# Kernel optimization log

Measured on AMD Instinct MI355X. Metric: run time of the kernel, lower is better.

Reference implementation:

```python
import jax, jax.numpy as jnp
import numpy as np
import math

B, N, E, L = 64, 2048, 8192, 50
IN_DIM, HID, HEADS, R, BASES = 128, 64, 3, 5, 4
NODE_NUM = 100000


def setup_inputs() -> dict:
    key = jax.random.key(0)
    ks = jax.random.split(key, 16)
    node_ids = jax.random.randint(ks[0], (B, N), 0, NODE_NUM)
    edge_index = jax.random.randint(ks[1], (B, 2, E), 0, N)
    edge_type = jax.random.randint(ks[2], (B, E), 0, R)
    sent_ids = jax.random.randint(ks[3], (B, L), 0, N)
    # embedding table, padding_idx=0 row zeroed, init N(0, 1/input_dim)
    emb_table = jax.random.normal(ks[4], (NODE_NUM, IN_DIM), jnp.float32) / IN_DIM
    emb_table = emb_table.at[0].set(0.0)
    # RGCN basis decomposition params
    bases = jax.random.normal(ks[5], (BASES, IN_DIM, IN_DIM), jnp.float32) * (1.0 / math.sqrt(IN_DIM))
    comp = jax.random.normal(ks[6], (R, BASES), jnp.float32) * 0.5
    root_w = jax.random.normal(ks[7], (IN_DIM, IN_DIM), jnp.float32) * (1.0 / math.sqrt(IN_DIM))
    root_b = jnp.zeros((IN_DIM,), jnp.float32)
    # attention weights: 3 heads concatenated along output dim -> [IN_DIM, 3*HID]
    xav = math.sqrt(6.0 / (IN_DIM + HID))
    wq = jax.random.uniform(ks[8], (IN_DIM, HEADS * HID), jnp.float32, -xav, xav)
    wk = jax.random.uniform(ks[9], (IN_DIM, HEADS * HID), jnp.float32, -xav, xav)
    wv = jax.random.uniform(ks[10], (IN_DIM, HEADS * HID), jnp.float32, -xav, xav)
    attn_w = jax.random.normal(ks[11], (HEADS * HID, 1), jnp.float32) * 0.05
    attn_b = jnp.zeros((1,), jnp.float32)
    fc_w = jax.random.normal(ks[12], (HEADS * HID, 1), jnp.float32) * 0.05
    fc_b = jnp.zeros((1,), jnp.float32)
    return {"emb_table": emb_table, "bases": bases, "comp": comp, "root_w": root_w,
            "root_b": root_b, "wq": wq, "wk": wk, "wv": wv, "attn_w": attn_w,
            "attn_b": attn_b, "fc_w": fc_w, "fc_b": fc_b, "node_ids": node_ids,
            "edge_index": edge_index, "edge_type": edge_type, "sent_ids": sent_ids}


def _rgcn_conv(x, ei, et, W, root_w, root_b):
    # x: [N, D], ei: [2, E], et: [E], W: [R, D, D]
    src, tgt = ei[0], ei[1]
    msg = jnp.einsum('ei,eio->eo', x[src], W[et])            # [E, D]
    # per-(target, relation) mean normalization (PyG RGCNConv default)
    key = tgt * R + et
    deg = jax.ops.segment_sum(jnp.ones((et.shape[0],), x.dtype), key, num_segments=N * R)
    norm = 1.0 / jnp.maximum(deg[key], 1.0)
    agg = jax.ops.segment_sum(msg * norm[:, None], tgt, num_segments=N)  # [N, D]
    return agg + x @ root_w + root_b


def reference(emb_table, bases, comp, root_w, root_b, wq, wk, wv,
              attn_w, attn_b, fc_w, fc_b, node_ids, edge_index, edge_type, sent_ids):
    # relation weights from basis decomposition: [R, D, D]
    W = jnp.einsum('rb,bio->rio', comp, bases)
    x = emb_table[node_ids]                                   # [B, N, D]
    x_upd = jax.vmap(_rgcn_conv, in_axes=(0, 0, 0, None, None, None))(
        x, edge_index, edge_type, W, root_w, root_b)          # [B, N, D]
    X = jnp.take_along_axis(x_upd, sent_ids[:, :, None], axis=1)  # [B, L, D]
    # self-attention with head-concatenated Q/K/V (single softmax over 3*HID dims)
    Q = X @ wq                                                # [B, L, 3H]
    K = X @ wk
    V = X @ wv
    scores = jax.nn.softmax(jnp.einsum('bld,bmd->blm', Q, K) / math.sqrt(HEADS * HID), axis=-1)
    H = jnp.einsum('blm,bmd->bld', scores, V)                 # [B, L, 3H]
    attn = H @ attn_w + attn_b                                # [B, L, 1]
    pooled = jnp.sum(H * attn, axis=1)                        # [B, 3H]
    return jax.nn.sigmoid(pooled @ fc_w + fc_b)               # [B, 1]
```

## Files before the change

### kernel.cpp

```cpp
#include <hip/hip_runtime.h>
#include <math.h>

#define BDIM 64
#define NN   2048
#define EE   8192
#define LL   50
#define DD   128
#define RR   5
#define NBASES 4
#define H3   192
#define RECCAP 1024
#define KDIM 768
#define GR   8

__device__ __forceinline__ void fma4(float4& a, float s, const float4& w) {
    a.x = fmaf(s, w.x, a.x); a.y = fmaf(s, w.y, a.y);
    a.z = fmaf(s, w.z, a.z); a.w = fmaf(s, w.w, a.w);
}

__global__ __launch_bounds__(256) void precompute_all(
        const float* __restrict__ bases, const float* __restrict__ comp,
        const float* __restrict__ root_w, const float* __restrict__ wq,
        const float* __restrict__ wk, const float* __restrict__ wv,
        const float* __restrict__ attn_w, const float* __restrict__ fc_w,
        float* __restrict__ Wcat, float* __restrict__ A,
        float* __restrict__ va, float* __restrict__ vf) {
    int blk = blockIdx.x, t = threadIdx.x;
    if (blk < 384) {
        int idx = blk * 256 + t;
        int k = idx >> 7, o = idx & 127;
        if (k < DD) {
            Wcat[idx] = root_w[idx];
        } else {
            int r = (k - DD) >> 7, i = (k - DD) & 127;
            float s = 0.f;
#pragma unroll
            for (int bb = 0; bb < NBASES; ++bb)
                s += comp[r * NBASES + bb] * bases[bb * DD * DD + i * DD + o];
            Wcat[idx] = s;
        }
    } else if (blk < 512) {
        int i = blk - 384;
        __shared__ float wqs[H3];
        if (t < H3) wqs[t] = wq[i * H3 + t];
        __syncthreads();
        if (t < DD) {
            const float4* wkr = (const float4*)(wk + t * H3);
            float s = 0.f;
#pragma unroll
            for (int d4 = 0; d4 < H3 / 4; ++d4) {
                float4 v = wkr[d4];
                s += wqs[4*d4]*v.x + wqs[4*d4+1]*v.y + wqs[4*d4+2]*v.z + wqs[4*d4+3]*v.w;
            }
            A[i * DD + t] = s;
        }
    } else {
        if (t < DD) {
            const float4* wr = (const float4*)(wv + t * H3);
            float a = 0.f, f = 0.f;
#pragma unroll
            for (int d4 = 0; d4 < H3 / 4; ++d4) {
                float4 v = wr[d4];
                a += v.x*attn_w[4*d4] + v.y*attn_w[4*d4+1] + v.z*attn_w[4*d4+2] + v.w*attn_w[4*d4+3];
                f += v.x*fc_w[4*d4] + v.y*fc_w[4*d4+1] + v.z*fc_w[4*d4+2] + v.w*fc_w[4*d4+3];
            }
            va[t] = a; vf[t] = f;
        }
    }
}

__global__ __launch_bounds__(512) void matchseg(const int* __restrict__ edge_index,
                                                const int* __restrict__ edge_type,
                                                const int* __restrict__ sent_ids,
                                                int* __restrict__ rep,
                                                int* __restrict__ segoff,
                                                int* __restrict__ recbuf2) {
    int b = blockIdx.x, t = threadIdx.x;
    __shared__ int mark[NN];
    __shared__ int scnt[LL * RR];
    __shared__ int soff[LL * RR + 1];
    __shared__ int scan[256];
    __shared__ int recs[RECCAP];
    __shared__ int lcnt;

    for (int i = t; i < NN; i += 512) mark[i] = -1;
    if (t < LL * RR) scnt[t] = 0;
    if (t == 0) lcnt = 0;
    __syncthreads();
    const int* sb = sent_ids + b * LL;
    if (t < LL) mark[sb[t]] = t;
    __syncthreads();
    if (t < LL) rep[b * LL + t] = mark[sb[t]];

    const int* src_arr = edge_index + (size_t)b * 2 * EE;
    const int* tgt_arr = src_arr + EE;
    const int* et_arr  = edge_type + (size_t)b * EE;
    const int4* tgt4 = (const int4*)tgt_arr;
    for (int i4 = t; i4 < EE / 4; i4 += 512) {
        int4 v = tgt4[i4];
        int e0 = 4 * i4;
        int lv[4] = {mark[v.x], mark[v.y], mark[v.z], mark[v.w]};
#pragma unroll
        for (int k = 0; k < 4; ++k) {
            int l = lv[k];
            if (l >= 0) {
                int e = e0 + k;
                int r = et_arr[e];
                int s = src_arr[e];
                int pos = atomicAdd(&lcnt, 1);
                if (pos < RECCAP) {
                    recs[pos] = (l << 14) | (r << 11) | s;
                    atomicAdd(&scnt[l * RR + r], 1);
                }
            }
        }
    }
    __syncthreads();
    if (t < 256) scan[t] = (t < LL * RR) ? scnt[t] : 0;
    __syncthreads();
    for (int off = 1; off < 256; off <<= 1) {
        int v = 0;
        if (t < 256 && t >= off) v = scan[t - off];
        __syncthreads();
        if (t < 256) scan[t] += v;
        __syncthreads();
    }
    if (t == 0) soff[0] = 0;
    if (t < LL * RR) soff[t + 1] = scan[t];
    if (t < LL * RR) scnt[t] = 0;
    __syncthreads();
    if (t <= LL * RR) segoff[b * (LL * RR + 1) + t] = soff[t];
    int nm = (lcnt < RECCAP) ? lcnt : RECCAP;
    for (int i = t; i < nm; i += 512) {
        int rc = recs[i];
        int key = (rc >> 14) * RR + ((rc >> 11) & 7);
        int pos = soff[key] + atomicAdd(&scnt[key], 1);
        recbuf2[b * RECCAP + pos] = rc;
    }
}

__global__ __launch_bounds__(256) void gemm_fused8(const float* __restrict__ emb,
                                                   const float* __restrict__ Wcat,
                                                   const float* __restrict__ A,
                                                   const float* __restrict__ root_b,
                                                   const float* __restrict__ va,
                                                   const float* __restrict__ vf,
                                                   const int* __restrict__ node_ids,
                                                   const int* __restrict__ sent_ids,
                                                   const int* __restrict__ rep,
                                                   const int* __restrict__ segoff,
                                                   const int* __restrict__ recbuf2,
                                                   float* __restrict__ Xws,
                                                   float* __restrict__ XAws,
                                                   float* __restrict__ pv,
                                                   float* __restrict__ qv) {
    __shared__ float Us[GR][KDIM];
    __shared__ float Xs[GR][DD];
    __shared__ float vas[DD], vfs[DD];

    int t = threadIdx.x;
    int w = t >> 6, lane = t & 63;
    int row0 = blockIdx.x * GR;

#pragma unroll
    for (int rr = 0; rr < 2; ++rr) {
        int lrow = 2 * w + rr;
        int bl = row0 + lrow;
        int b  = bl / LL;
        const int* nid = node_ids + (size_t)b * NN;
        int myrep = rep[bl];
        const int* so = segoff + b * (LL * RR + 1) + myrep * RR;
        const int* rb = recbuf2 + b * RECCAP;
        int nrow = nid[sent_ids[bl]];
        Us[lrow][lane]      = emb[(size_t)nrow * DD + lane];
        Us[lrow][lane + 64] = emb[(size_t)nrow * DD + 64 + lane];
#pragma unroll
        for (int r = 0; r < RR; ++r) {
            int s0 = so[r], s1 = so[r + 1];
            float a0 = 0.f, a1 = 0.f;
            for (int j = s0; j < s1; ++j) {
                int s = rb[j] & 2047;
                int rw = nid[s];
                a0 += emb[(size_t)rw * DD + lane];
                a1 += emb[(size_t)rw * DD + 64 + lane];
            }
            float inv = (s1 > s0) ? 1.f / (float)(s1 - s0) : 0.f;
            Us[lrow][DD + r * DD + lane]      = a0 * inv;
            Us[lrow][DD + r * DD + 64 + lane] = a1 * inv;
        }
    }
    if (t < DD) { vas[t] = va[t]; vfs[t] = vf[t]; }
    __syncthreads();

    int cg = t & 31, rg = t >> 5;
    int bl_r = row0 + rg;
    float4 acc = *(const float4*)(root_b + 4 * cg);
    const float4* Wc4 = (const float4*)Wcat;
    const float4* u4p = (const float4*)Us[rg];
#pragma unroll 2
    for (int k4 = 0; k4 < KDIM / 4; ++k4) {
        float4 u = u4p[k4];
        int k = 4 * k4;
        float4 w0 = Wc4[(k + 0) * 32 + cg];
        float4 w1 = Wc4[(k + 1) * 32 + cg];
        float4 w2 = Wc4[(k + 2) * 32 + cg];
        float4 w3 = Wc4[(k + 3) * 32 + cg];
        fma4(acc, u.x, w0);
        fma4(acc, u.y, w1);
        fma4(acc, u.z, w2);
        fma4(acc, u.w, w3);
    }
    *(float4*)&Xs[rg][4 * cg] = acc;
    *(float4*)(Xws + (size_t)bl_r * DD + 4 * cg) = acc;

    float4 z = {0.f, 0.f, 0.f, 0.f};
    const float4* A4 = (const float4*)A;
    const float4* x4p = (const float4*)Xs[rg];
#pragma unroll 2
    for (int k4 = 0; k4 < DD / 4; ++k4) {
        float4 x = x4p[k4];
        int k = 4 * k4;
        float4 a0 = A4[(k + 0) * 32 + cg];
        float4 a1 = A4[(k + 1) * 32 + cg];
        float4 a2 = A4[(k + 2) * 32 + cg];
        float4 a3 = A4[(k + 3) * 32 + cg];
        fma4(z, x.x, a0);
        fma4(z, x.y, a1);
        fma4(z, x.z, a2);
        fma4(z, x.w, a3);
    }
    *(float4*)(XAws + (size_t)bl_r * DD + 4 * cg) = z;

#pragma unroll
    for (int rr = 0; rr < 2; ++rr) {
        int m = 2 * w + rr;
        float xv0 = Xs[m][lane], xv1 = Xs[m][lane + 64];
        float pp = xv0 * vas[lane] + xv1 * vas[lane + 64];
        float qq = xv0 * vfs[lane] + xv1 * vfs[lane + 64];
#pragma unroll
        for (int off = 32; off; off >>= 1) {
            pp += __shfl_xor(pp, off);
            qq += __shfl_xor(qq, off);
        }
        if (lane == 0) { pv[row0 + m] = pp; qv[row0 + m] = qq; }
    }
}

__global__ __launch_bounds__(256) void attn_batch(const float* __restrict__ Xws,
                                                  const float* __restrict__ XAws,
                                                  const float* __restrict__ pv,
                                                  const float* __restrict__ qv,
                                                  const float* __restrict__ attn_b,
                                                  const float* __restrict__ fc_b,
                                                  float* __restrict__ out) {
    __shared__ float4 XT4[32][64];
    __shared__ float4 XA4[LL][32];
    __shared__ float pvs[64], qvs[64];
    __shared__ float partial[4];

    int b = blockIdx.x, t = threadIdx.x;
    int w = t >> 6, lane = t & 63;

    const float4* Xb4  = (const float4*)(Xws  + (size_t)b * LL * DD);
    const float4* XAb4 = (const float4*)(XAws + (size_t)b * LL * DD);
    for (int idx = t; idx < LL * 32; idx += 256) {
        int m = idx >> 5, k = idx & 31;
        XT4[k][m] = Xb4[idx];
        ((float4*)XA4)[idx] = XAb4[idx];
    }
    if (t < 64) {
        pvs[t] = (t < LL) ? pv[b * LL + t] : 0.f;
        qvs[t] = (t < LL) ? qv[b * LL + t] : 0.f;
    }
    __syncthreads();

    const float scale = 0.07216878364870322f;
    float ab = attn_b[0];
    float local = 0.f;
    for (int l = w; l < LL; l += 4) {
        float s = 0.f;
#pragma unroll
        for (int kk = 0; kk < 32; ++kk) {
            float4 xa = XA4[l][kk];
            float4 xt = XT4[kk][lane];
            s = fmaf(xa.x, xt.x, s);
            s = fmaf(xa.y, xt.y, s);
            s = fmaf(xa.z, xt.z, s);
            s = fmaf(xa.w, xt.w, s);
        }
        s *= scale;
        float sval = (lane < LL) ? s : -INFINITY;
        float mx = sval;
#pragma unroll
        for (int off = 32; off; off >>= 1) mx = fmaxf(mx, __shfl_xor(mx, off));
        float e = (lane < LL) ? __expf(sval - mx) : 0.f;
        float sum = e, pa = e * pvs[lane], qa = e * qvs[lane];
#pragma unroll
        for (int off = 32; off; off >>= 1) {
            sum += __shfl_xor(sum, off);
            pa  += __shfl_xor(pa, off);
            qa  += __shfl_xor(qa, off);
        }
        float inv = 1.f / sum;
        local += (pa * inv + ab) * (qa * inv);
    }
    if (lane == 0) partial[w] = local;
    __syncthreads();
    if (t == 0) {
        float s = partial[0] + partial[1] + partial[2] + partial[3];
        out[b] = 1.f / (1.f + expf(-(s + fc_b[0])));
    }
}

extern "C" void kernel_launch(void* const* d_in, const int* in_sizes, int n_in,
                              void* d_out, int out_size, void* d_ws, size_t ws_size,
                              hipStream_t stream) {
    const float* emb     = (const float*)d_in[0];
    const float* bases   = (const float*)d_in[1];
    const float* comp    = (const float*)d_in[2];
    const float* root_w  = (const float*)d_in[3];
    const float* root_b  = (const float*)d_in[4];
    const float* wq      = (const float*)d_in[5];
    const float* wk      = (const float*)d_in[6];
    const float* wv      = (const float*)d_in[7];
    const float* attn_w  = (const float*)d_in[8];
    const float* attn_b  = (const float*)d_in[9];
    const float* fc_w    = (const float*)d_in[10];
    const float* fc_b    = (const float*)d_in[11];
    const int* node_ids  = (const int*)d_in[12];
    const int* edge_index= (const int*)d_in[13];
    const int* edge_type = (const int*)d_in[14];
    const int* sent_ids  = (const int*)d_in[15];
    float* out = (float*)d_out;

    float* ws = (float*)d_ws;
    float* Wcat = ws;
    float* A    = ws + 98304;
    float* va   = ws + 114688;
    float* vf   = ws + 114816;
    float* pv   = ws + 114944;
    float* qv   = ws + 118144;
    float* Xws  = ws + 121344;
    float* XAws = ws + 530944;
    int* rep     = (int*)(ws + 940544);
    int* segoff  = (int*)(ws + 943744);
    int* recbuf2 = (int*)(ws + 959808);

    hipLaunchKernelGGL(precompute_all, dim3(513), dim3(256), 0, stream,
                       bases, comp, root_w, wq, wk, wv, attn_w, fc_w,
                       Wcat, A, va, vf);
    hipLaunchKernelGGL(matchseg, dim3(BDIM), dim3(512), 0, stream,
                       edge_index, edge_type, sent_ids, rep, segoff, recbuf2);
    hipLaunchKernelGGL(gemm_fused8, dim3(BDIM * LL / GR), dim3(256), 0, stream,
                       emb, Wcat, A, root_b, va, vf, node_ids, sent_ids,
                       rep, segoff, recbuf2, Xws, XAws, pv, qv);
    hipLaunchKernelGGL(attn_batch, dim3(BDIM), dim3(256), 0, stream,
                       Xws, XAws, pv, qv, attn_b, fc_b, out);
}
```

Before: 207.8 us.

## Fold XA projection into weights and split GEMM over K with smem tiling

```diff
diff --git a/kernel.cpp b/kernel.cpp
--- a/kernel.cpp
+++ b/kernel.cpp
@@ -10,35 +10,40 @@
 #define NBASES 4
 #define H3   192
 #define RECCAP 1024
-#define KDIM 768
-#define GR   8
+#define MT   16
+#define NS   3
+#define SK   256
+#define KC   32
 
 __device__ __forceinline__ void fma4(float4& a, float s, const float4& w) {
     a.x = fmaf(s, w.x, a.x); a.y = fmaf(s, w.y, a.y);
     a.z = fmaf(s, w.z, a.z); a.w = fmaf(s, w.w, a.w);
 }
 
-__global__ __launch_bounds__(256) void precompute_all(
+__global__ __launch_bounds__(256) void precompute_base(
         const float* __restrict__ bases, const float* __restrict__ comp,
-        const float* __restrict__ root_w, const float* __restrict__ wq,
-        const float* __restrict__ wk, const float* __restrict__ wv,
-        const float* __restrict__ attn_w, const float* __restrict__ fc_w,
-        float* __restrict__ Wcat, float* __restrict__ A,
-        float* __restrict__ va, float* __restrict__ vf) {
+        const float* __restrict__ root_w, const float* __restrict__ root_b,
+        const float* __restrict__ wq, const float* __restrict__ wk,
+        const float* __restrict__ wv, const float* __restrict__ attn_w,
+        const float* __restrict__ fc_w,
+        float* __restrict__ W2, float* __restrict__ A,
+        float* __restrict__ va, float* __restrict__ vf,
+        float* __restrict__ bias2) {
     int blk = blockIdx.x, t = threadIdx.x;
     if (blk < 384) {
         int idx = blk * 256 + t;
         int k = idx >> 7, o = idx & 127;
+        float s;
         if (k < DD) {
-            Wcat[idx] = root_w[idx];
+            s = root_w[idx];
         } else {
             int r = (k - DD) >> 7, i = (k - DD) & 127;
-            float s = 0.f;
+            s = 0.f;
 #pragma unroll
             for (int bb = 0; bb < NBASES; ++bb)
                 s += comp[r * NBASES + bb] * bases[bb * DD * DD + i * DD + o];
-            Wcat[idx] = s;
-        }
+        }
+        W2[(size_t)k * 256 + o] = s;
     } else if (blk < 512) {
         int i = blk - 384;
         __shared__ float wqs[H3];
@@ -65,7 +70,28 @@
                 f += v.x*fc_w[4*d4] + v.y*fc_w[4*d4+1] + v.z*fc_w[4*d4+2] + v.w*fc_w[4*d4+3];
             }
             va[t] = a; vf[t] = f;
-        }
+            bias2[t] = root_b[t];
+        }
+    }
+}
+
+__global__ __launch_bounds__(128) void precompute_fold(
+        const float* __restrict__ A, const float* __restrict__ root_b,
+        float* __restrict__ W2, float* __restrict__ bias2) {
+    int i = blockIdx.x, j = threadIdx.x;
+    __shared__ float wrow[DD];
+    if (i < 768) {
+        wrow[j] = W2[(size_t)i * 256 + j];
+        __syncthreads();
+        float s = 0.f;
+        for (int k = 0; k < DD; ++k) s = fmaf(wrow[k], A[k * DD + j], s);
+        W2[(size_t)i * 256 + 128 + j] = s;
+    } else {
+        wrow[j] = root_b[j];
+        __syncthreads();
+        float s = 0.f;
+        for (int k = 0; k < DD; ++k) s = fmaf(wrow[k], A[k * DD + j], s);
+        bias2[128 + j] = s;
     }
 }
 
@@ -139,138 +165,146 @@
     }
 }
 
-__global__ __launch_bounds__(256) void gemm_fused8(const float* __restrict__ emb,
-                                                   const float* __restrict__ Wcat,
-                                                   const float* __restrict__ A,
-                                                   const float* __restrict__ root_b,
-                                                   const float* __restrict__ va,
-                                                   const float* __restrict__ vf,
+__global__ __launch_bounds__(256) void gemm_ksplit(const float* __restrict__ emb,
+                                                   const float* __restrict__ W2,
                                                    const int* __restrict__ node_ids,
                                                    const int* __restrict__ sent_ids,
                                                    const int* __restrict__ rep,
                                                    const int* __restrict__ segoff,
                                                    const int* __restrict__ recbuf2,
-                                                   float* __restrict__ Xws,
-                                                   float* __restrict__ XAws,
-                                                   float* __restrict__ pv,
-                                                   float* __restrict__ qv) {
-    __shared__ float Us[GR][KDIM];
-    __shared__ float Xs[GR][DD];
-    __shared__ float vas[DD], vfs[DD];
+                                                   float* __restrict__ Xpart) {
+    __shared__ float Uc[MT][SK];
+    __shared__ float Wb[KC][256];
 
     int t = threadIdx.x;
     int w = t >> 6, lane = t & 63;
-    int row0 = blockIdx.x * GR;
-
-#pragma unroll
-    for (int rr = 0; rr < 2; ++rr) {
-        int lrow = 2 * w + rr;
-        int bl = row0 + lrow;
+    int mt = blockIdx.x % 200;
+    int ks = blockIdx.x / 200;
+    int m0 = mt * MT;
+
+#pragma unroll
+    for (int rr = 0; rr < 4; ++rr) {
+        int row = 4 * w + rr;
+        int bl = m0 + row;
         int b  = bl / LL;
         const int* nid = node_ids + (size_t)b * NN;
         int myrep = rep[bl];
         const int* so = segoff + b * (LL * RR + 1) + myrep * RR;
         const int* rb = recbuf2 + b * RECCAP;
-        int nrow = nid[sent_ids[bl]];
-        Us[lrow][lane]      = emb[(size_t)nrow * DD + lane];
-        Us[lrow][lane + 64] = emb[(size_t)nrow * DD + 64 + lane];
-#pragma unroll
-        for (int r = 0; r < RR; ++r) {
-            int s0 = so[r], s1 = so[r + 1];
-            float a0 = 0.f, a1 = 0.f;
-            for (int j = s0; j < s1; ++j) {
-                int s = rb[j] & 2047;
-                int rw = nid[s];
-                a0 += emb[(size_t)rw * DD + lane];
-                a1 += emb[(size_t)rw * DD + 64 + lane];
-            }
-            float inv = (s1 > s0) ? 1.f / (float)(s1 - s0) : 0.f;
-            Us[lrow][DD + r * DD + lane]      = a0 * inv;
-            Us[lrow][DD + r * DD + 64 + lane] = a1 * inv;
-        }
-    }
-    if (t < DD) { vas[t] = va[t]; vfs[t] = vf[t]; }
-    __syncthreads();
-
-    int cg = t & 31, rg = t >> 5;
-    int bl_r = row0 + rg;
-    float4 acc = *(const float4*)(root_b + 4 * cg);
-    const float4* Wc4 = (const float4*)Wcat;
-    const float4* u4p = (const float4*)Us[rg];
-#pragma unroll 2
-    for (int k4 = 0; k4 < KDIM / 4; ++k4) {
-        float4 u = u4p[k4];
-        int k = 4 * k4;
-        float4 w0 = Wc4[(k + 0) * 32 + cg];
-        float4 w1 = Wc4[(k + 1) * 32 + cg];
-        float4 w2 = Wc4[(k + 2) * 32 + cg];
-        float4 w3 = Wc4[(k + 3) * 32 + cg];
-        fma4(acc, u.x, w0);
-        fma4(acc, u.y, w1);
-        fma4(acc, u.z, w2);
-        fma4(acc, u.w, w3);
-    }
-    *(float4*)&Xs[rg][4 * cg] = acc;
-    *(float4*)(Xws + (size_t)bl_r * DD + 4 * cg) = acc;
-
-    float4 z = {0.f, 0.f, 0.f, 0.f};
-    const float4* A4 = (const float4*)A;
-    const float4* x4p = (const float4*)Xs[rg];
-#pragma unroll 2
-    for (int k4 = 0; k4 < DD / 4; ++k4) {
-        float4 x = x4p[k4];
-        int k = 4 * k4;
-        float4 a0 = A4[(k + 0) * 32 + cg];
-        float4 a1 = A4[(k + 1) * 32 + cg];
-        float4 a2 = A4[(k + 2) * 32 + cg];
-        float4 a3 = A4[(k + 3) * 32 + cg];
-        fma4(z, x.x, a0);
-        fma4(z, x.y, a1);
-        fma4(z, x.z, a2);
-        fma4(z, x.w, a3);
-    }
-    *(float4*)(XAws + (size_t)bl_r * DD + 4 * cg) = z;
-
-#pragma unroll
-    for (int rr = 0; rr < 2; ++rr) {
-        int m = 2 * w + rr;
-        float xv0 = Xs[m][lane], xv1 = Xs[m][lane + 64];
-        float pp = xv0 * vas[lane] + xv1 * vas[lane + 64];
-        float qq = xv0 * vfs[lane] + xv1 * vfs[lane + 64];
-#pragma unroll
-        for (int off = 32; off; off >>= 1) {
-            pp += __shfl_xor(pp, off);
-            qq += __shfl_xor(qq, off);
-        }
-        if (lane == 0) { pv[row0 + m] = pp; qv[row0 + m] = qq; }
-    }
-}
-
-__global__ __launch_bounds__(256) void attn_batch(const float* __restrict__ Xws,
-                                                  const float* __restrict__ XAws,
-                                                  const float* __restrict__ pv,
-                                                  const float* __restrict__ qv,
+#pragma unroll
+        for (int s = 0; s < 2; ++s) {
+            int kind = ks * 2 + s - 1;
+            float u0, u1;
+            if (kind < 0) {
+                int nrow = nid[sent_ids[bl]];
+                u0 = emb[(size_t)nrow * DD + lane];
+                u1 = emb[(size_t)nrow * DD + 64 + lane];
+            } else {
+                int s0 = so[kind], s1 = so[kind + 1];
+                float a0 = 0.f, a1 = 0.f;
+                for (int j = s0; j < s1; ++j) {
+                    int sv = rb[j] & 2047;
+                    int rw = nid[sv];
+                    a0 += emb[(size_t)rw * DD + lane];
+                    a1 += emb[(size_t)rw * DD + 64 + lane];
+                }
+                float inv = (s1 > s0) ? 1.f / (float)(s1 - s0) : 0.f;
+                u0 = a0 * inv; u1 = a1 * inv;
+            }
+            Uc[row][s * DD + lane]      = u0;
+            Uc[row][s * DD + 64 + lane] = u1;
+        }
+    }
+    __syncthreads();
+
+    int cg = lane;
+    float4 acc0 = {0,0,0,0}, acc1 = {0,0,0,0}, acc2 = {0,0,0,0}, acc3 = {0,0,0,0};
+    const float4* W2_4 = (const float4*)W2;
+    int kbase = ks * SK;
+    for (int c = 0; c < SK / KC; ++c) {
+        __syncthreads();
+        for (int it = 0; it < KC * 256 / 4 / 256; ++it) {
+            int fid = it * 256 + t;
+            int kr = fid >> 6, col4 = fid & 63;
+            ((float4*)Wb)[fid] = W2_4[(size_t)(kbase + c * KC + kr) * 64 + col4];
+        }
+        __syncthreads();
+        int kb = c * KC;
+#pragma unroll 4
+        for (int kk = 0; kk < KC; ++kk) {
+            float4 wv = ((const float4*)Wb[kk])[cg];
+            float u0 = Uc[4 * w + 0][kb + kk];
+            float u1 = Uc[4 * w + 1][kb + kk];
+            float u2 = Uc[4 * w + 2][kb + kk];
+            float u3 = Uc[4 * w + 3][kb + kk];
+            fma4(acc0, u0, wv);
+            fma4(acc1, u1, wv);
+            fma4(acc2, u2, wv);
+            fma4(acc3, u3, wv);
+        }
+    }
+    size_t base = ((size_t)ks * 3200 + m0 + 4 * w) * 256 + 4 * cg;
+    *(float4*)(Xpart + base)           = acc0;
+    *(float4*)(Xpart + base + 256)     = acc1;
+    *(float4*)(Xpart + base + 512)     = acc2;
+    *(float4*)(Xpart + base + 768)     = acc3;
+}
+
+__global__ __launch_bounds__(256) void attn_batch(const float* __restrict__ Xpart,
+                                                  const float* __restrict__ bias2,
+                                                  const float* __restrict__ va,
+                                                  const float* __restrict__ vf,
                                                   const float* __restrict__ attn_b,
                                                   const float* __restrict__ fc_b,
                                                   float* __restrict__ out) {
     __shared__ float4 XT4[32][64];
     __shared__ float4 XA4[LL][32];
     __shared__ float pvs[64], qvs[64];
+    __shared__ float4 va4[32], vf4[32];
     __shared__ float partial[4];
 
     int b = blockIdx.x, t = threadIdx.x;
     int w = t >> 6, lane = t & 63;
 
-    const float4* Xb4  = (const float4*)(Xws  + (size_t)b * LL * DD);
-    const float4* XAb4 = (const float4*)(XAws + (size_t)b * LL * DD);
-    for (int idx = t; idx < LL * 32; idx += 256) {
-        int m = idx >> 5, k = idx & 31;
-        XT4[k][m] = Xb4[idx];
-        ((float4*)XA4)[idx] = XAb4[idx];
-    }
-    if (t < 64) {
-        pvs[t] = (t < LL) ? pv[b * LL + t] : 0.f;
-        qvs[t] = (t < LL) ? qv[b * LL + t] : 0.f;
+    const float4* bias4 = (const float4*)bias2;
+    for (int idx = t; idx < LL * 64; idx += 256) {
+        int row = idx >> 6, c4 = idx & 63;
+        float4 v = bias4[c4];
+        size_t p0 = ((size_t)b * LL + row) * 64 + c4;
+#pragma unroll
+        for (int ks = 0; ks < NS; ++ks) {
+            float4 xp = ((const float4*)Xpart)[(size_t)ks * 3200 * 64 + p0];
+            v.x += xp.x; v.y += xp.y; v.z += xp.z; v.w += xp.w;
+        }
+        if (c4 < 32) XT4[c4][row] = v;
+        else         XA4[row][c4 - 32] = v;
+    }
+    if (t < 32) va4[t] = ((const float4*)va)[t];
+    else if (t < 64) vf4[t - 32] = ((const float4*)vf)[t - 32];
+    __syncthreads();
+
+    if (w == 0) {
+        float s = 0.f;
+        if (lane < LL) {
+#pragma unroll
+            for (int kk = 0; kk < 32; ++kk) {
+                float4 x = XT4[kk][lane], vv = va4[kk];
+                s = fmaf(x.x, vv.x, s); s = fmaf(x.y, vv.y, s);
+                s = fmaf(x.z, vv.z, s); s = fmaf(x.w, vv.w, s);
+            }
+        }
+        pvs[lane] = s;
+    } else if (w == 1) {
+        float s = 0.f;
+        if (lane < LL) {
+#pragma unroll
+            for (int kk = 0; kk < 32; ++kk) {
+                float4 x = XT4[kk][lane], vv = vf4[kk];
+                s = fmaf(x.x, vv.x, s); s = fmaf(x.y, vv.y, s);
+                s = fmaf(x.z, vv.z, s); s = fmaf(x.w, vv.w, s);
+            }
+        }
+        qvs[lane] = s;
     }
     __syncthreads();
 
@@ -334,26 +368,25 @@
     float* out = (float*)d_out;
 
     float* ws = (float*)d_ws;
-    float* Wcat = ws;
-    float* A    = ws + 98304;
-    float* va   = ws + 114688;
-    float* vf   = ws + 114816;
-    float* pv   = ws + 114944;
-    float* qv   = ws + 118144;
-    float* Xws  = ws + 121344;
-    float* XAws = ws + 530944;
-    int* rep     = (int*)(ws + 940544);
-    int* segoff  = (int*)(ws + 943744);
-    int* recbuf2 = (int*)(ws + 959808);
-
-    hipLaunchKernelGGL(precompute_all, dim3(513), dim3(256), 0, stream,
-                       bases, comp, root_w, wq, wk, wv, attn_w, fc_w,
-                       Wcat, A, va, vf);
+    float* W2    = ws;
+    float* A     = ws + 196608;
+    float* bias2 = ws + 212992;
+    float* va    = ws + 213248;
+    float* vf    = ws + 213376;
+    float* Xpart = ws + 213504;
+    int* rep     = (int*)(ws + 2671104);
+    int* segoff  = (int*)(ws + 2674304);
+    int* recbuf2 = (int*)(ws + 2690368);
+
+    hipLaunchKernelGGL(precompute_base, dim3(513), dim3(256), 0, stream,
+                       bases, comp, root_w, root_b, wq, wk, wv, attn_w, fc_w,
+                       W2, A, va, vf, bias2);
+    hipLaunchKernelGGL(precompute_fold, dim3(769), dim3(128), 0, stream,
+                       A, root_b, W2, bias2);
     hipLaunchKernelGGL(matchseg, dim3(BDIM), dim3(512), 0, stream,
                        edge_index, edge_type, sent_ids, rep, segoff, recbuf2);
-    hipLaunchKernelGGL(gemm_fused8, dim3(BDIM * LL / GR), dim3(256), 0, stream,
-                       emb, Wcat, A, root_b, va, vf, node_ids, sent_ids,
-                       rep, segoff, recbuf2, Xws, XAws, pv, qv);
+    hipLaunchKernelGGL(gemm_ksplit, dim3(200 * NS), dim3(256), 0, stream,
+                       emb, W2, node_ids, sent_ids, rep, segoff, recbuf2, Xpart);
     hipLaunchKernelGGL(attn_batch, dim3(BDIM), dim3(256), 0, stream,
-                       Xws, XAws, pv, qv, attn_b, fc_b, out);
-}
+                       Xpart, bias2, va, vf, attn_b, fc_b, out);
+}
```

Measured after the change: 184.8 us. 11.1% less time.
